# Kernel optimization log

Measured on AMD Instinct MI355X. Metric: run time of the kernel, lower is better.

The kernel has to match this reference:

```python
import jax, jax.numpy as jnp
import numpy as np

N = 200000      # nodes
E = 12_800_000  # edges
G = 512         # graphs in batch
D = 2           # point_dim


def setup_inputs() -> dict:
    key = jax.random.key(0)
    ks = jax.random.split(key, 12)
    x = jax.random.normal(ks[0], (N, D), dtype=jnp.float32)
    edge_index = jax.random.randint(ks[1], (2, E), 0, N, dtype=jnp.int64)
    batch = jnp.sort(jax.random.randint(ks[2], (N,), 0, G, dtype=jnp.int64))
    s = 0.5
    W1 = jax.random.normal(ks[3], (D, 2), dtype=jnp.float32) * s
    b1 = jax.random.normal(ks[4], (2,), dtype=jnp.float32) * 0.1
    W2 = jax.random.normal(ks[5], (2, 2), dtype=jnp.float32) * s
    b2 = jax.random.normal(ks[6], (2,), dtype=jnp.float32) * 0.1
    W3 = jax.random.normal(ks[7], (2, 2), dtype=jnp.float32) * s
    b3 = jax.random.normal(ks[8], (2,), dtype=jnp.float32) * 0.1
    Wr = jax.random.normal(ks[9], (2, 1), dtype=jnp.float32) * s
    br = jax.random.normal(ks[10], (1,), dtype=jnp.float32) * 0.1
    return {"x": x, "edge_index": edge_index, "batch": batch,
            "W1": W1, "b1": b1, "W2": W2, "b2": b2,
            "W3": W3, "b3": b3, "Wr": Wr, "br": br}


def _gcn_conv(x, W, b, src, dst, norm, n_nodes):
    # PyG GCNConv: h = x @ W; out_i = sum_j norm_ij * h_j (incl. self-loops) + b
    h = x @ W
    agg = jax.ops.segment_sum(h[src] * norm[:, None], dst, num_segments=n_nodes)
    return agg + b


def reference(x, edge_index, batch, W1, b1, W2, b2, W3, b3, Wr, br):
    n = x.shape[0]
    loop = jnp.arange(n, dtype=edge_index.dtype)
    # GCNConv adds self-loops; same edge_index for all layers, so do it once.
    src = jnp.concatenate([edge_index[0], loop])
    dst = jnp.concatenate([edge_index[1], loop])
    # symmetric normalization: deg from target nodes (incl self-loops)
    deg = jax.ops.segment_sum(jnp.ones(dst.shape[0], x.dtype), dst, num_segments=n)
    dinv = jnp.where(deg > 0, jax.lax.rsqrt(deg), 0.0)
    norm = dinv[src] * dinv[dst]

    h = jax.nn.relu(_gcn_conv(x, W1, b1, src, dst, norm, n))
    h = jax.nn.relu(_gcn_conv(h, W2, b2, src, dst, norm, n))
    h = jax.nn.relu(_gcn_conv(h, W3, b3, src, dst, norm, n))
    pooled = jax.ops.segment_sum(h, batch, num_segments=G)  # global_add_pool -> [G, 2]
    return (pooled @ Wr + br)[:, 0]  # squeeze(1) -> [G]
```

## Files before the change

### kernel.cpp

```cpp
#include <hip/hip_runtime.h>

#define BLK 256
#define BLK2 1024
#define BSHIFT 8
#define BSIZE 256
#define NSLICE 256
#define SCAN_T 1024
#define KPAD 1024
#define EPT 8
#define TILE2 (BLK2 * EPT)
#define S2BLK 1024
#define S2CAP 18432
#define S2MAXJ 18

typedef int iv4 __attribute__((ext_vector_type(4)));

template <typename T>
__device__ __forceinline__ T ntload(const T* p) { return __builtin_nontemporal_load(p); }

__device__ __forceinline__ iv4 ntload4(const int* p) {
    return __builtin_nontemporal_load((const iv4*)p);
}

template <int CTRL>
__device__ __forceinline__ float dpp_add(float v) {
    int t = __builtin_amdgcn_update_dpp(0, __float_as_int(v), CTRL, 0xf, 0xf, true);
    return v + __int_as_float(t);
}
__device__ __forceinline__ float wave_sum63(float v) {
    v = dpp_add<0x111>(v);
    v = dpp_add<0x112>(v);
    v = dpp_add<0x114>(v);
    v = dpp_add<0x118>(v);
    v = dpp_add<0x142>(v);
    v = dpp_add<0x143>(v);
    return v;
}


__global__ void __launch_bounds__(BLK2) k_hist(const int* __restrict__ dst,
                                               int* __restrict__ partial,
                                               int E, int chunk, int K) {
    extern __shared__ int cnt[];
    int s = blockIdx.x;
    for (int i = threadIdx.x; i < K; i += BLK2) cnt[i] = 0;
    __syncthreads();
    int lo = s * chunk, hi = min(E, lo + chunk);
    int a0 = min((lo + 3) & ~3, hi);
    int a1 = max(hi & ~3, a0);
    for (int i = lo + threadIdx.x; i < a0; i += BLK2)
        atomicAdd(&cnt[((unsigned)ntload(dst + i)) >> BSHIFT], 1);
    for (int i = a0 + 4 * threadIdx.x; i < a1; i += 4 * BLK2) {
        iv4 q = ntload4(dst + i);
        atomicAdd(&cnt[((unsigned)q.x) >> BSHIFT], 1);
        atomicAdd(&cnt[((unsigned)q.y) >> BSHIFT], 1);
        atomicAdd(&cnt[((unsigned)q.z) >> BSHIFT], 1);
        atomicAdd(&cnt[((unsigned)q.w) >> BSHIFT], 1);
    }
    for (int i = a1 + threadIdx.x; i < hi; i += BLK2)
        atomicAdd(&cnt[((unsigned)ntload(dst + i)) >> BSHIFT], 1);
    __syncthreads();
    int* prow = partial + (size_t)s * K;
    for (int i = threadIdx.x; i < K; i += BLK2) prow[i] = cnt[i];
}

__global__ void __launch_bounds__(NSLICE) k_colscan(int* __restrict__ partial,
                                                    int* __restrict__ totals, int K) {
    __shared__ int sh[NSLICE];
    int k = blockIdx.x;
    int t = threadIdx.x;
    int v = partial[(size_t)t * K + k];
    sh[t] = v;
    __syncthreads();
    for (int off = 1; off < NSLICE; off <<= 1) {
        int u = (t >= off) ? sh[t - off] : 0;
        __syncthreads();
        sh[t] += u;
        __syncthreads();
    }
    partial[(size_t)t * K + k] = sh[t] - v;
    if (t == NSLICE - 1) totals[k] = sh[t];
}

__global__ void __launch_bounds__(SCAN_T) k_base(const int* __restrict__ totals,
                                                 int* __restrict__ base, int K) {
    __shared__ int sh[SCAN_T];
    int t = threadIdx.x;
    int v = (t < K) ? totals[t] : 0;
    sh[t] = v;
    __syncthreads();
    for (int off = 1; off < SCAN_T; off <<= 1) {
        int u = (t >= off) ? sh[t - off] : 0;
        __syncthreads();
        sh[t] += u;
        __syncthreads();
    }
    if (t < K) base[t + 1] = sh[t];
    if (t == 0) base[0] = 0;
}

__global__ void __launch_bounds__(BLK2) k_scatter(const int* __restrict__ src,
                                                  const int* __restrict__ dst,
                                                  const int* __restrict__ offs,
                                                  const int* __restrict__ base,
                                                  int* __restrict__ packed,
                                                  int E, int chunk, int K, int sbits) {
    __shared__ int cnt[KPAD];
    __shared__ int cur[KPAD];
    __shared__ int gstart[KPAD];
    __shared__ int tsum[KPAD];
    __shared__ int sval[TILE2];
    __shared__ int sadr[TILE2];
    int s = blockIdx.x;
    int tid = threadIdx.x;
    const int* orow = offs + (size_t)s * K;
    cur[tid] = (tid < K) ? orow[tid] + base[tid] : 0;
    int lo = s * chunk, hi = min(E, lo + chunk);

    for (int tlo = lo; tlo < hi; tlo += TILE2) {
        cnt[tid] = 0;
        __syncthreads();

        int kk[EPT], rr[EPT], vv[EPT];
#pragma unroll
        for (int j = 0; j < EPT; ++j) {
            int i = tlo + j * BLK2 + tid;
            kk[j] = -1;
            if (i < hi) {
                int d = ntload(dst + i);
                int sc = ntload(src + i);
                kk[j] = ((unsigned)d) >> BSHIFT;
                vv[j] = ((d & (BSIZE - 1)) << sbits) | sc;
                rr[j] = atomicAdd(&cnt[kk[j]], 1);
            }
        }
        __syncthreads();

        int c = cnt[tid];
        tsum[tid] = c;
        __syncthreads();
        for (int off = 1; off < KPAD; off <<= 1) {
            int u = (tid >= off) ? tsum[tid - off] : 0;
            __syncthreads();
            tsum[tid] += u;
            __syncthreads();
        }
        int excl = tsum[tid] - c;
        gstart[tid] = cur[tid];
        cur[tid] += c;
        cnt[tid] = excl;
        __syncthreads();

#pragma unroll
        for (int j = 0; j < EPT; ++j) {
            if (kk[j] >= 0) {
                int idx = cnt[kk[j]] + rr[j];
                sval[idx] = vv[j];
                sadr[idx] = gstart[kk[j]] + rr[j];
            }
        }
        __syncthreads();

        int tot = min(hi - tlo, TILE2);
        for (int i2 = tid; i2 < tot; i2 += BLK2)
            packed[sadr[i2]] = sval[i2];
        __syncthreads();
    }
}

__global__ void __launch_bounds__(S2BLK) k_sort2(const int* __restrict__ packed,
                                                 const int* __restrict__ base,
                                                 int* __restrict__ packed2,
                                                 int* __restrict__ rowptr,
                                                 int sbits, int K, int E) {
    __shared__ int cnt[BSIZE];
    __shared__ int sc[BSIZE];
    __shared__ int startsh[BSIZE];
    __shared__ int cur[BSIZE];
    extern __shared__ int sorted[];
    int k = blockIdx.x;
    int tid = threadIdx.x;
    int lo = base[k], hi = base[k + 1];
    int len = hi - lo;
    bool fits = (len <= S2CAP);

    if (tid < BSIZE) cnt[tid] = 0;
    __syncthreads();

    int v[S2MAXJ], r[S2MAXJ];
    if (fits) {
#pragma unroll
        for (int j = 0; j < S2MAXJ; ++j) {
            int i = lo + j * S2BLK + tid;
            r[j] = -1;
            if (i < hi) {
                v[j] = ntload(packed + i);
                r[j] = atomicAdd(&cnt[((unsigned)v[j]) >> sbits], 1);
            }
        }
    } else {
        for (int i = lo + tid; i < hi; i += S2BLK)
            atomicAdd(&cnt[((unsigned)ntload(packed + i)) >> sbits], 1);
    }
    __syncthreads();

    if (tid < BSIZE) sc[tid] = cnt[tid];
    __syncthreads();
    for (int off = 1; off < BSIZE; off <<= 1) {
        int u = 0;
        if (tid < BSIZE && tid >= off) u = sc[tid - off];
        __syncthreads();
        if (tid < BSIZE) sc[tid] += u;
        __syncthreads();
    }
    if (tid < BSIZE) {
        int st = sc[tid] - cnt[tid];
        startsh[tid] = st;
        cur[tid] = lo + st;
        rowptr[(k << BSHIFT) + tid] = lo + st;
    }
    if (k == K - 1 && tid == 0) rowptr[K << BSHIFT] = E;
    __syncthreads();

    if (fits) {
#pragma unroll
        for (int j = 0; j < S2MAXJ; ++j) {
            if (r[j] >= 0)
                sorted[startsh[((unsigned)v[j]) >> sbits] + r[j]] = v[j];
        }
        __syncthreads();
        for (int i = tid; i < len; i += S2BLK)
            __builtin_nontemporal_store(sorted[i], packed2 + lo + i);
    } else {
        for (int i = lo + tid; i < hi; i += S2BLK) {
            int val = ntload(packed + i);
            int pos = atomicAdd(&cur[((unsigned)val) >> sbits], 1);
            packed2[pos] = val;
        }
    }
}


__global__ void __launch_bounds__(BLK) k_agg4(const int* __restrict__ edges,
                                              const int* __restrict__ rowptr,
                                              const float* __restrict__ dinv,
                                              const float2* __restrict__ pin,
                                              const float* __restrict__ b,
                                              const float* __restrict__ W,
                                              float2* __restrict__ pout,
                                              int N, int smask) {
    int wid = threadIdx.x >> 6, lane = threadIdx.x & 63;
    int n = blockIdx.x * 4 + wid;
    if (n >= N) return;
    int e0 = rowptr[n], e1 = rowptr[n + 1];
    float sx = 0.f, sy = 0.f;
    for (int i = e0 + lane; i < e1; i += 64) {
        float2 e = pin[((unsigned)edges[i]) & smask];
        sx += e.x;
        sy += e.y;
    }
    sx = wave_sum63(sx);
    sy = wave_sum63(sy);
    if (lane == 63) {
        float di = dinv[n];
        float2 self = pin[n];
        float ax = sx + self.x, ay = sy + self.y;
        float h0 = fmaxf(fmaf(di, ax, b[0]), 0.f);
        float h1 = fmaxf(fmaf(di, ay, b[1]), 0.f);
        pout[n] = make_float2(di * (h0 * W[0] + h1 * W[2]),
                              di * (h0 * W[1] + h1 * W[3]));
    }
}

__global__ void __launch_bounds__(BLK) k_agg4f(const int* __restrict__ edges,
                                               const int* __restrict__ rowptr,
                                               const float* __restrict__ dinv,
                                               const float2* __restrict__ pin,
                                               const float* __restrict__ b,
                                               const float* __restrict__ Wr,
                                               float* __restrict__ sv,
                                               int N, int smask) {
    int wid = threadIdx.x >> 6, lane = threadIdx.x & 63;
    int n = blockIdx.x * 4 + wid;
    if (n >= N) return;
    int e0 = rowptr[n], e1 = rowptr[n + 1];
    float sx = 0.f, sy = 0.f;
    for (int i = e0 + lane; i < e1; i += 64) {
        float2 e = pin[((unsigned)edges[i]) & smask];
        sx += e.x;
        sy += e.y;
    }
    sx = wave_sum63(sx);
    sy = wave_sum63(sy);
    if (lane == 63) {
        float di = dinv[n];
        float2 self = pin[n];
        float ax = sx + self.x, ay = sy + self.y;
        float h0 = fmaxf(fmaf(di, ax, b[0]), 0.f);
        float h1 = fmaxf(fmaf(di, ay, b[1]), 0.f);
        sv[n] = fmaf(h0, Wr[0], h1 * Wr[1]);
    }
}


__global__ void k_node1(const int* __restrict__ rowptr, const float* __restrict__ x,
                        const float* __restrict__ W1, float* __restrict__ dinv,
                        float2* __restrict__ p1, int N) {
    int i = blockIdx.x * BLK + threadIdx.x;
    if (i >= N) return;
    int deg = rowptr[i + 1] - rowptr[i];
    float di = rsqrtf((float)deg + 1.0f);
    dinv[i] = di;
    float2 xv = ((const float2*)x)[i];
    float w00 = W1[0], w01 = W1[1], w10 = W1[2], w11 = W1[3];
    p1[i] = make_float2(di * (xv.x * w00 + xv.y * w10),
                        di * (xv.x * w01 + xv.y * w11));
}

__global__ void k_out_init(float* __restrict__ out, const float* __restrict__ br, int G) {
    int i = blockIdx.x * BLK + threadIdx.x;
    if (i < G) out[i] = br[0];
}

__global__ void k_pool(const float* __restrict__ sv, const int* __restrict__ batch,
                       float* __restrict__ out, int N) {
    int i = blockIdx.x * BLK + threadIdx.x;
    bool valid = i < N;
    float s = valid ? sv[i] : 0.f;
    int key = valid ? batch[i] : -1;
    int lane = threadIdx.x & 63;
    for (int off = 1; off < 64; off <<= 1) {
        float s2 = __shfl_down(s, off);
        int k2 = __shfl_down(key, off);
        if (lane + off < 64 && k2 == key) s += s2;
    }
    int kprev = __shfl_up(key, 1);
    if (valid && (lane == 0 || kprev != key)) unsafeAtomicAdd(&out[key], s);
}


extern "C" void kernel_launch(void* const* d_in, const int* in_sizes, int n_in,
                              void* d_out, int out_size, void* d_ws, size_t ws_size,
                              hipStream_t stream) {
    const float* x    = (const float*)d_in[0];
    const int*   ei   = (const int*)d_in[1];
    const int*   batch= (const int*)d_in[2];
    const float* W1   = (const float*)d_in[3];
    const float* b1   = (const float*)d_in[4];
    const float* W2   = (const float*)d_in[5];
    const float* b2   = (const float*)d_in[6];
    const float* W3   = (const float*)d_in[7];
    const float* b3   = (const float*)d_in[8];
    const float* Wr   = (const float*)d_in[9];
    const float* br   = (const float*)d_in[10];
    float* out = (float*)d_out;

    int N = in_sizes[0] / 2;
    int E = in_sizes[1] / 2;
    int G = out_size;
    const int* src = ei;
    const int* dst = ei + E;

    int K = (N + BSIZE - 1) >> BSHIFT;
    if (K > KPAD) return;
    int S = NSLICE;
    int chunk = (E + S - 1) / S;

    int sbits = 1;
    while ((1 << sbits) < N) ++sbits;
    if (sbits + BSHIFT > 31) return;
    int smask = (1 << sbits) - 1;

    auto pad16 = [](size_t b) { return (b + 15) & ~(size_t)15; };
    size_t need = pad16((size_t)E * 4)
                + pad16((size_t)S * K * 4)
                + pad16((size_t)(K + 1) * 4)
                + pad16((size_t)K * 4)
                + pad16((size_t)E * 4)
                + pad16(((size_t)K * BSIZE + 1) * 4)
                + pad16((size_t)N * 4)
                + 2 * pad16((size_t)N * 8)
                + pad16((size_t)N * 4);
    if (need > ws_size) return;

    char* w = (char*)d_ws;
    size_t off = 0;
    auto carve = [&](size_t bytes) { void* p = w + off; off += (bytes + 15) & ~(size_t)15; return p; };
    int*    packed  = (int*)carve((size_t)E * 4);
    int*    hpart   = (int*)carve((size_t)S * K * 4);
    int*    basep   = (int*)carve((size_t)(K + 1) * 4);
    int*    totals  = (int*)carve((size_t)K * 4);
    int*    packed2 = (int*)carve((size_t)E * 4);
    int*    rowptr  = (int*)carve(((size_t)K * BSIZE + 1) * 4);
    float*  dinv    = (float*)carve((size_t)N * 4);
    float2* pA      = (float2*)carve((size_t)N * 8);
    float2* pB      = (float2*)carve((size_t)N * 8);
    float*  sv      = (float*)carve((size_t)N * 4);

    int NB = (N + BLK - 1) / BLK;
    int GB = (G + BLK - 1) / BLK;
    int WB = (N + 3) / 4;
    size_t smemK = (size_t)K * 4;

    k_hist   <<<S, BLK2, smemK, stream>>>(dst, hpart, E, chunk, K);
    k_colscan<<<K, NSLICE, 0, stream>>>(hpart, totals, K);
    k_base   <<<1, SCAN_T, 0, stream>>>(totals, basep, K);
    k_scatter<<<S, BLK2, 0, stream>>>(src, dst, hpart, basep, packed, E, chunk, K, sbits);

    k_sort2  <<<K, S2BLK, (size_t)S2CAP * 4, stream>>>(packed, basep, packed2, rowptr,
                                                       sbits, K, E);

    k_node1  <<<NB, BLK, 0, stream>>>(rowptr, x, W1, dinv, pA, N);

    k_agg4   <<<WB, BLK, 0, stream>>>(packed2, rowptr, dinv, pA, b1, W2, pB, N, smask);
    k_agg4   <<<WB, BLK, 0, stream>>>(packed2, rowptr, dinv, pB, b2, W3, pA, N, smask);
    k_agg4f  <<<WB, BLK, 0, stream>>>(packed2, rowptr, dinv, pA, b3, Wr, sv, N, smask);

    k_out_init<<<GB, BLK, 0, stream>>>(out, br, G);
    k_pool    <<<NB, BLK, 0, stream>>>(sv, batch, out, N);
}
```

Measured before the change: 365.2 us.

## Buffer partial 64-byte runs per bucket in LDS to align scatter writes

The radix scatter kernel now holds, for each bucket, the trailing elements that do not fill a 16-int (64-byte) aligned segment in a per-bucket LDS residue buffer. They are flushed once the segment fills on a later tile, or at kernel end. Global writes from each tile then cover only whole aligned segments, which should reduce partial-line write traffic. The cost is extra LDS (K*64 bytes), serial per-thread flush loops, and more branching in the placement loop.

```diff
diff --git a/kernel.cpp b/kernel.cpp
--- a/kernel.cpp
+++ b/kernel.cpp
@@ -106,15 +106,19 @@
                                                   int* __restrict__ packed,
                                                   int E, int chunk, int K, int sbits) {
     __shared__ int cnt[KPAD];
+    __shared__ int tsum[KPAD];
+    __shared__ int gstart[KPAD];
+    __shared__ int fesh[KPAD];
     __shared__ int cur[KPAD];
-    __shared__ int gstart[KPAD];
-    __shared__ int tsum[KPAD];
+    __shared__ int res[KPAD];
     __shared__ int sval[TILE2];
     __shared__ int sadr[TILE2];
+    extern __shared__ int resbuf[];
     int s = blockIdx.x;
     int tid = threadIdx.x;
     const int* orow = offs + (size_t)s * K;
     cur[tid] = (tid < K) ? orow[tid] + base[tid] : 0;
+    res[tid] = 0;
     int lo = s * chunk, hi = min(E, lo + chunk);
 
     for (int tlo = lo; tlo < hi; tlo += TILE2) {
@@ -145,26 +149,50 @@
             tsum[tid] += u;
             __syncthreads();
         }
-        int excl = tsum[tid] - c;
-        gstart[tid] = cur[tid];
-        cur[tid] += c;
-        cnt[tid] = excl;
+        if (tid < K) {
+            int cur_old = cur[tid];
+            int res_old = res[tid];
+            int ds = cur_old - res_old;
+            int fe = (cur_old + c) & ~15;
+            int flushHi = min(fe, cur_old);
+            for (int p = ds; p < flushHi; ++p)
+                packed[p] = resbuf[tid * 16 + (p & 15)];
+            res[tid] = (cur_old + c) - max(fe, ds);
+            cur[tid] = cur_old + c;
+            fesh[tid] = fe;
+            gstart[tid] = cur_old;
+        }
+        cnt[tid] = tsum[tid] - c;
         __syncthreads();
 
 #pragma unroll
         for (int j = 0; j < EPT; ++j) {
             if (kk[j] >= 0) {
                 int idx = cnt[kk[j]] + rr[j];
+                int pos = gstart[kk[j]] + rr[j];
                 sval[idx] = vv[j];
-                sadr[idx] = gstart[kk[j]] + rr[j];
+                if (pos < fesh[kk[j]]) {
+                    sadr[idx] = pos;
+                } else {
+                    sadr[idx] = -1;
+                    resbuf[kk[j] * 16 + (pos & 15)] = vv[j];
+                }
             }
         }
         __syncthreads();
 
         int tot = min(hi - tlo, TILE2);
-        for (int i2 = tid; i2 < tot; i2 += BLK2)
-            packed[sadr[i2]] = sval[i2];
-        __syncthreads();
+        for (int i2 = tid; i2 < tot; i2 += BLK2) {
+            int a2 = sadr[i2];
+            if (a2 >= 0) packed[a2] = sval[i2];
+        }
+        __syncthreads();
+    }
+
+    if (tid < K) {
+        int cu = cur[tid], re = res[tid];
+        for (int p = cu - re; p < cu; ++p)
+            packed[p] = resbuf[tid * 16 + (p & 15)];
     }
 }
 
@@ -405,7 +433,8 @@
     k_hist   <<<S, BLK2, smemK, stream>>>(dst, hpart, E, chunk, K);
     k_colscan<<<K, NSLICE, 0, stream>>>(hpart, totals, K);
     k_base   <<<1, SCAN_T, 0, stream>>>(totals, basep, K);
-    k_scatter<<<S, BLK2, 0, stream>>>(src, dst, hpart, basep, packed, E, chunk, K, sbits);
+    k_scatter<<<S, BLK2, (size_t)K * 16 * 4, stream>>>(src, dst, hpart, basep, packed,
+                                                       E, chunk, K, sbits);
 
     k_sort2  <<<K, S2BLK, (size_t)S2CAP * 4, stream>>>(packed, basep, packed2, rowptr,
                                                        sbits, K, E);
```

After: 371.9 us. Within noise of the previous version (+1.9%).
